# Optimization experiments

Measured on AMD Instinct MI355X. Metric: run time of the kernel, lower is better.

The kernel has to match this reference:

```python
import jax, jax.numpy as jnp
import numpy as np

TOP_K = 2

def setup_inputs() -> dict:
    key = jax.random.key(0)
    ks = jax.random.split(key, 8)
    B, T, C, E, I, S = 1, 2048, 2048, 8, 1408, 2816
    s = 0.02  # weight scale for numerical stability
    return {
        "x": jax.random.normal(ks[0], (B, T, C), jnp.float32),
        "gate_w": jax.random.normal(ks[1], (E, C), jnp.float32) * s,
        "w1": jax.random.normal(ks[2], (E, I, C), jnp.float32) * s,
        "w3": jax.random.normal(ks[3], (E, I, C), jnp.float32) * s,
        "w2": jax.random.normal(ks[4], (E, C, I), jnp.float32) * s,
        "sw1": jax.random.normal(ks[5], (S, C), jnp.float32) * s,
        "sw3": jax.random.normal(ks[6], (S, C), jnp.float32) * s,
        "sw2": jax.random.normal(ks[7], (C, S), jnp.float32) * s,
    }

def reference(x, gate_w, w1, w3, w2, sw1, sw3, sw2):
    B, T, C = x.shape
    E = gate_w.shape[0]
    xf = x.reshape(-1, C)                      # [N, C]
    N = xf.shape[0]
    # --- routing: top-k of raw logits, softmax over the k selected logits ---
    logits = xf @ gate_w.T                     # [N, E]
    pv, idx = jax.lax.top_k(logits, TOP_K)     # [N, K]
    pv = jax.nn.softmax(pv.astype(jnp.float32), axis=-1).astype(x.dtype)
    # token-expert combine weights (sum of probs per expert, scatter of top-k)
    tew = jnp.zeros((N, E), x.dtype).at[jnp.arange(N)[:, None], idx].add(pv)
    # --- experts (SwiGLU), computed densely over all experts and masked by tew ---
    h = jax.nn.silu(jnp.einsum('nc,eic->nei', xf, w1)) * jnp.einsum('nc,eic->nei', xf, w3)
    eo = jnp.einsum('nei,eci->nec', h, w2)     # [N, E, C]
    y = jnp.einsum('nec,ne->nc', eo, tew).reshape(B, T, C)
    # --- shared expert on the residual input ---
    sh = (jax.nn.silu(x @ sw1.T) * (x @ sw3.T)) @ sw2.T
    return y + sh
```

## Files before the change

### kernel.cpp

```cpp
#include <hip/hip_runtime.h>

#define DEVI __device__ __forceinline__

typedef __attribute__((ext_vector_type(4))) float f32x4;
typedef __attribute__((ext_vector_type(8))) short bf16x8;

static constexpr int NT = 2048;
static constexpr int CD = 2048;
static constexpr int NE = 8;
static constexpr int ID = 1408;
static constexpr int SD = 2816;
static constexpr int ROWS = 2 * NT;
static constexpr int ROWS_PAD = ROWS + 128;

DEVI unsigned short f2bf(float f) {
  unsigned u = __builtin_bit_cast(unsigned, f);
  u += 0x7fff + ((u >> 16) & 1);
  return (unsigned short)(u >> 16);
}
DEVI float bf2f(unsigned short s) { return __builtin_bit_cast(float, (unsigned)s << 16); }
DEVI float silu_f(float z) { return z / (1.f + __expf(-z)); }

DEVI void gll16(const void* g, void* l) {
  __builtin_amdgcn_global_load_lds((__attribute__((address_space(1))) void*)(void*)g,
                                   (__attribute__((address_space(3))) void*)l, 16, 0, 0);
}

DEVI void bar_sched() {
  __builtin_amdgcn_s_barrier();
  __builtin_amdgcn_sched_barrier(0);
}
DEVI void wait_vm8() { asm volatile("s_waitcnt vmcnt(8)" ::: "memory"); }
DEVI void wait_vm0() { asm volatile("s_waitcnt vmcnt(0)" ::: "memory"); }
DEVI void wait_lgk0() { asm volatile("s_waitcnt lgkmcnt(0)" ::: "memory"); }

DEVI int swz_chunk(int bid, int nwg) {
  constexpr int CH = 16, G = 8 * CH;
  int nfull = nwg - (nwg % G);
  if (bid >= nfull) return bid;
  int c = bid / G, r = bid % G;
  return c * G + (r % 8) * CH + (r / 8);
}

__global__ __launch_bounds__(256) void k_cvt(const float* __restrict__ s,
                                             unsigned short* __restrict__ d, int n8)
{
  int i = blockIdx.x * 256 + threadIdx.x;
  int stride = gridDim.x * 256;
  for (; i < n8; i += stride) {
    float4 a = ((const float4*)s)[2 * i];
    float4 b = ((const float4*)s)[2 * i + 1];
    ushort4 p0 = make_ushort4(f2bf(a.x), f2bf(a.y), f2bf(a.z), f2bf(a.w));
    ushort4 p1 = make_ushort4(f2bf(b.x), f2bf(b.y), f2bf(b.z), f2bf(b.w));
    ((ushort4*)d)[2 * i]     = p0;
    ((ushort4*)d)[2 * i + 1] = p1;
  }
}

__global__ __launch_bounds__(64) void k_router(const float* __restrict__ x,
    const float* __restrict__ gw, int* __restrict__ counts,
    int* __restrict__ eidx, int* __restrict__ posn, float* __restrict__ probs)
{
  const int n = blockIdx.x;
  const int lane = threadIdx.x;
  const float4* xr = (const float4*)(x + (size_t)n * CD);
  float acc[NE];
#pragma unroll
  for (int e = 0; e < NE; ++e) acc[e] = 0.f;
  for (int i = lane; i < CD / 4; i += 64) {
    float4 xv = xr[i];
#pragma unroll
    for (int e = 0; e < NE; ++e) {
      float4 gv = ((const float4*)(gw + (size_t)e * CD))[i];
      acc[e] += xv.x * gv.x + xv.y * gv.y + xv.z * gv.z + xv.w * gv.w;
    }
  }
#pragma unroll
  for (int e = 0; e < NE; ++e) {
    float v = acc[e];
#pragma unroll
    for (int off = 32; off > 0; off >>= 1) v += __shfl_down(v, off);
    acc[e] = v;
  }
  if (lane == 0) {
    int b0 = 0; float m0 = acc[0];
#pragma unroll
    for (int e = 1; e < NE; ++e) if (acc[e] > m0) { m0 = acc[e]; b0 = e; }
    int b1 = -1; float m1 = 0.f;
#pragma unroll
    for (int e = 0; e < NE; ++e) {
      if (e == b0) continue;
      if (b1 < 0 || acc[e] > m1) { m1 = acc[e]; b1 = e; }
    }
    float d = __expf(m1 - m0);
    float inv = 1.f / (1.f + d);
    eidx[2 * n] = b0; eidx[2 * n + 1] = b1;
    probs[2 * n] = inv; probs[2 * n + 1] = d * inv;
    posn[2 * n] = atomicAdd(&counts[b0], 1);
    posn[2 * n + 1] = atomicAdd(&counts[b1], 1);
  }
}

__global__ void k_scan(const int* __restrict__ counts, int* __restrict__ bases) {
  if (threadIdx.x == 0) {
    int s = 0;
    for (int e = 0; e < NE; ++e) { bases[e] = s; s += counts[e]; }
  }
}

__global__ __launch_bounds__(256) void k_build(const int* __restrict__ eidx,
    const int* __restrict__ posn, const int* __restrict__ bases,
    int* __restrict__ rows_of, int* __restrict__ row2tok)
{
  int n = blockIdx.x * 256 + threadIdx.x;
  if (n >= NT) return;
#pragma unroll
  for (int k = 0; k < 2; ++k) {
    int e = eidx[2 * n + k];
    int row = bases[e] + posn[2 * n + k];
    rows_of[2 * n + k] = row;
    row2tok[row] = n;
  }
}

struct GArgs {
  const unsigned short* A;
  const unsigned short* B1; const unsigned short* B3;
  void* Out;
  const int* counts; const int* bases; const int* row2tok;
  const int* rows_of; const float* probs; const unsigned short* eo;
};

template<int MODE>
__global__ __launch_bounds__(256) void k_gemm(GArgs a)
{
  constexpr bool DUAL = (MODE == 0 || MODE == 2);
  constexpr int KD = (MODE == 0 || MODE == 2) ? CD : (MODE == 1 ? ID : SD);
  constexpr int BN = DUAL ? 64 : 128;
  constexpr int NH = BN / 2;
  constexpr int NFT = NH / 16;
  constexpr int BT = DUAL ? 2 : 4;
  constexpr int NMB = NT / 128;
  constexpr int NPN = (MODE == 0) ? ID / 64 : (MODE == 2) ? SD / 64 : CD / 128;
  constexpr int NWG = NMB * NPN * ((MODE <= 1) ? NE : 1);
  constexpr int NSTEP = KD / 64;

  __shared__ __align__(16) char sm[2][32768];

  int lin = swz_chunk((int)blockIdx.x, NWG);
  const int mx = lin % NMB; lin /= NMB;
  const int pn = lin % NPN;
  const int e  = lin / NPN;

  int M, baserow = 0;
  if constexpr (MODE <= 1) {
    int ne = a.counts[e];
    if (mx * 128 >= ne) return;
    M = ne; baserow = a.bases[e];
  } else { M = NT; }
  const int m0 = mx * 128;
  const int n0 = pn * BN;

  const unsigned short* B1;
  const unsigned short* B3 = nullptr;
  if constexpr (MODE == 0)      { B1 = a.B1 + ((size_t)e * ID + n0) * CD; B3 = a.B3 + ((size_t)e * ID + n0) * CD; }
  else if constexpr (MODE == 1) { B1 = a.B1 + ((size_t)e * CD + n0) * ID; }
  else if constexpr (MODE == 2) { B1 = a.B1 + (size_t)n0 * CD; B3 = a.B3 + (size_t)n0 * CD; }
  else                          { B1 = a.B1 + (size_t)n0 * SD; }

  const int tid = threadIdx.x, l = tid & 63, w = tid >> 6;
  const int wr = w >> 1, wc = w & 1;
  const int slot = ((l & 7) ^ ((l >> 3) & 7)) * 16;

  const char* aP[4];
#pragma unroll
  for (int t = 0; t < 4; ++t) {
    int r = w * 32 + t * 8 + (l >> 3);
    const unsigned short* rb;
    if constexpr (MODE == 0) {
      int grow = m0 + r; int gr = grow < M ? grow : 0;
      rb = a.A + (size_t)a.row2tok[baserow + gr] * CD;
    } else if constexpr (MODE == 1) {
      rb = a.A + (size_t)(baserow + m0 + r) * KD;
    } else {
      rb = a.A + (size_t)(m0 + r) * KD;
    }
    aP[t] = (const char*)rb + slot;
  }
  const char* bP1[BT]; const char* bP3[BT];
#pragma unroll
  for (int t = 0; t < BT; ++t) {
    int r = w * (8 * BT) + t * 8 + (l >> 3);
    bP1[t] = (const char*)(B1 + (size_t)r * KD) + slot;
    if constexpr (DUAL) bP3[t] = (const char*)(B3 + (size_t)r * KD) + slot;
  }

  f32x4 acc1[4][NFT]; f32x4 acc3[4][NFT];
#pragma unroll
  for (int m = 0; m < 4; ++m)
#pragma unroll
    for (int n = 0; n < NFT; ++n) {
      acc1[m][n] = {0.f, 0.f, 0.f, 0.f};
      if constexpr (DUAL) acc3[m][n] = {0.f, 0.f, 0.f, 0.f};
    }

  const int lrow = l & 15, lkg = l >> 4, l7 = l & 7;
  const int ao0 = (lkg ^ l7) * 16;
  const int ao1 = ((4 + lkg) ^ l7) * 16;

  auto stageF = [&](char* base, size_t kb) {
    char* sA = base; char* sB1 = base + 16384; char* sB3 = base + 24576;
#pragma unroll
    for (int t = 0; t < 4; ++t) gll16(aP[t] + kb, sA + (w * 4 + t) * 1024);
#pragma unroll
    for (int t = 0; t < BT; ++t) {
      gll16(bP1[t] + kb, sB1 + (w * BT + t) * 1024);
      if constexpr (DUAL) gll16(bP3[t] + kb, sB3 + (w * BT + t) * 1024);
    }
  };
  auto computeF = [&](const char* base) {
    const char* sA = base; const char* sB1 = base + 16384; const char* sB3 = base + 24576;
#pragma unroll
    for (int kk = 0; kk < 2; ++kk) {
      const int ao = kk ? ao1 : ao0;
      bf16x8 af[4];
#pragma unroll
      for (int m = 0; m < 4; ++m)
        af[m] = *(const bf16x8*)(sA + (wr * 64 + m * 16 + lrow) * 128 + ao);
#pragma unroll
      for (int n = 0; n < NFT; ++n) {
        bf16x8 b1 = *(const bf16x8*)(sB1 + (wc * NH + n * 16 + lrow) * 128 + ao);
        bf16x8 b3;
        if constexpr (DUAL)
          b3 = *(const bf16x8*)(sB3 + (wc * NH + n * 16 + lrow) * 128 + ao);
#pragma unroll
        for (int m = 0; m < 4; ++m) {
          acc1[m][n] = __builtin_amdgcn_mfma_f32_16x16x32_bf16(af[m], b1, acc1[m][n], 0, 0, 0);
          if constexpr (DUAL)
            acc3[m][n] = __builtin_amdgcn_mfma_f32_16x16x32_bf16(af[m], b3, acc3[m][n], 0, 0, 0);
        }
      }
    }
  };

  stageF(sm[0], 0);
  int t = 0;
  for (; t < NSTEP - 2; t += 2) {
    stageF(sm[1], (size_t)(t + 1) * 128);
    wait_vm8(); bar_sched();
    computeF(sm[0]);
    wait_lgk0(); bar_sched();
    stageF(sm[0], (size_t)(t + 2) * 128);
    wait_vm8(); bar_sched();
    computeF(sm[1]);
    wait_lgk0(); bar_sched();
  }
  stageF(sm[1], (size_t)(NSTEP - 1) * 128);
  wait_vm8(); bar_sched();
  computeF(sm[0]);
  wait_vm0(); bar_sched();
  computeF(sm[1]);

#pragma unroll
  for (int m = 0; m < 4; ++m) {
    int rbase = m0 + wr * 64 + m * 16 + lkg * 4;
#pragma unroll
    for (int j = 0; j < 4; ++j) {
      int grow = rbase + j;
      if constexpr (MODE <= 1) { if (grow >= M) continue; }
      int r0 = 0, r1 = 0; float p0 = 0.f, p1 = 0.f;
      if constexpr (MODE == 3) {
        r0 = a.rows_of[2 * grow]; r1 = a.rows_of[2 * grow + 1];
        p0 = a.probs[2 * grow];   p1 = a.probs[2 * grow + 1];
      }
#pragma unroll
      for (int n = 0; n < NFT; ++n) {
        int gcol = n0 + wc * NH + n * 16 + lrow;
        float v1 = acc1[m][n][j];
        if constexpr (MODE == 0) {
          float hh = silu_f(v1) * acc3[m][n][j];
          ((unsigned short*)a.Out)[(size_t)(baserow + grow) * ID + gcol] = f2bf(hh);
        } else if constexpr (MODE == 1) {
          ((unsigned short*)a.Out)[(size_t)(baserow + grow) * CD + gcol] = f2bf(v1);
        } else if constexpr (MODE == 2) {
          float hh = silu_f(v1) * acc3[m][n][j];
          ((unsigned short*)a.Out)[(size_t)grow * SD + gcol] = f2bf(hh);
        } else {
          float vv = v1 + p0 * bf2f(a.eo[(size_t)r0 * CD + gcol]) + p1 * bf2f(a.eo[(size_t)r1 * CD + gcol]);
          ((float*)a.Out)[(size_t)grow * CD + gcol] = vv;
        }
      }
    }
  }
}

extern "C" void kernel_launch(void* const* d_in, const int* in_sizes, int n_in,
                              void* d_out, int out_size, void* d_ws, size_t ws_size,
                              hipStream_t stream)
{
  const float* x   = (const float*)d_in[0];
  const float* gw  = (const float*)d_in[1];
  const float* w1  = (const float*)d_in[2];
  const float* w3  = (const float*)d_in[3];
  const float* w2  = (const float*)d_in[4];
  const float* sw1 = (const float*)d_in[5];
  const float* sw3 = (const float*)d_in[6];
  const float* sw2 = (const float*)d_in[7];
  float* y = (float*)d_out;

  char* p = (char*)d_ws;
  auto alloc = [&](size_t b) { char* r = p; p += (b + 255) & ~(size_t)255; return r; };
  int*   counts  = (int*)alloc(NE * 4);
  int*   bases   = (int*)alloc(NE * 4);
  int*   eidx    = (int*)alloc((size_t)NT * 2 * 4);
  int*   posn    = (int*)alloc((size_t)NT * 2 * 4);
  float* probs   = (float*)alloc((size_t)NT * 2 * 4);
  int*   rows_of = (int*)alloc((size_t)NT * 2 * 4);
  int*   row2tok = (int*)alloc((size_t)ROWS * 4);
  unsigned short* xb   = (unsigned short*)alloc((size_t)NT * CD * 2);
  unsigned short* w1b  = (unsigned short*)alloc((size_t)NE * ID * CD * 2);
  unsigned short* w3b  = (unsigned short*)alloc((size_t)NE * ID * CD * 2);
  unsigned short* w2b  = (unsigned short*)alloc((size_t)NE * CD * ID * 2);
  unsigned short* sw1b = (unsigned short*)alloc((size_t)SD * CD * 2);
  unsigned short* sw3b = (unsigned short*)alloc((size_t)SD * CD * 2);
  unsigned short* sw2b = (unsigned short*)alloc((size_t)CD * SD * 2);
  unsigned short* h    = (unsigned short*)alloc((size_t)ROWS_PAD * ID * 2);
  unsigned short* eo   = (unsigned short*)alloc((size_t)ROWS_PAD * CD * 2);
  unsigned short* hs   = (unsigned short*)alloc((size_t)NT * SD * 2);

  hipMemsetAsync(counts, 0, NE * 4, stream);

  auto cvt = [&](const float* s, unsigned short* d, size_t n) {
    int n8 = (int)(n / 8);
    int grid = (n8 + 255) / 256; if (grid > 2048) grid = 2048;
    k_cvt<<<grid, 256, 0, stream>>>(s, d, n8);
  };
  cvt(x,   xb,   (size_t)NT * CD);
  cvt(w1,  w1b,  (size_t)NE * ID * CD);
  cvt(w3,  w3b,  (size_t)NE * ID * CD);
  cvt(w2,  w2b,  (size_t)NE * CD * ID);
  cvt(sw1, sw1b, (size_t)SD * CD);
  cvt(sw3, sw3b, (size_t)SD * CD);
  cvt(sw2, sw2b, (size_t)CD * SD);

  k_router<<<NT, 64, 0, stream>>>(x, gw, counts, eidx, posn, probs);
  k_scan<<<1, 64, 0, stream>>>(counts, bases);
  k_build<<<NT / 256, 256, 0, stream>>>(eidx, posn, bases, rows_of, row2tok);

  {
    GArgs g{}; g.A = xb; g.B1 = sw1b; g.B3 = sw3b; g.Out = hs;
    k_gemm<2><<<(NT / 128) * (SD / 64), 256, 0, stream>>>(g);
  }
  {
    GArgs g{}; g.A = xb; g.B1 = w1b; g.B3 = w3b; g.Out = h;
    g.counts = counts; g.bases = bases; g.row2tok = row2tok;
    k_gemm<0><<<(NT / 128) * (ID / 64) * NE, 256, 0, stream>>>(g);
  }
  {
    GArgs g{}; g.A = h; g.B1 = w2b; g.Out = eo;
    g.counts = counts; g.bases = bases;
    k_gemm<1><<<(NT / 128) * (CD / 128) * NE, 256, 0, stream>>>(g);
  }
  {
    GArgs g{}; g.A = hs; g.B1 = sw2b; g.Out = y;
    g.rows_of = rows_of; g.probs = probs; g.eo = eo;
    k_gemm<3><<<(NT / 128) * (CD / 128), 256, 0, stream>>>(g);
  }
}
```

Baseline: 401.2 us.

## Merge shared and routed GEMMs into grouped kernels with 256-row tiles

Replaces the four per-mode GEMM launches with two grouped kernels. One handles the shared and routed up-projections together, the other the down-projections. Tiles grow to 256 rows with 512 threads and 128 KB of dynamic LDS, and a separate combine kernel adds the weighted expert outputs into y. The aim is more data reuse per tile, one wave of mixed work to fill the CUs, and less launch and tail overhead. In exchange, expert tiles padded to 256 rows waste more compute, and the extra combine pass rereads y and eo.

```diff
diff --git a/kernel.cpp b/kernel.cpp
--- a/kernel.cpp
+++ b/kernel.cpp
@@ -11,7 +11,7 @@
 static constexpr int ID = 1408;
 static constexpr int SD = 2816;
 static constexpr int ROWS = 2 * NT;
-static constexpr int ROWS_PAD = ROWS + 128;
+static constexpr int ROWS_PAD = ROWS + 256;
 
 DEVI unsigned short f2bf(float f) {
   unsigned u = __builtin_bit_cast(unsigned, f);
@@ -34,8 +34,8 @@
 DEVI void wait_vm0() { asm volatile("s_waitcnt vmcnt(0)" ::: "memory"); }
 DEVI void wait_lgk0() { asm volatile("s_waitcnt lgkmcnt(0)" ::: "memory"); }
 
-DEVI int swz_chunk(int bid, int nwg) {
-  constexpr int CH = 16, G = 8 * CH;
+DEVI int swz8(int bid, int nwg) {
+  constexpr int CH = 8, G = 64;
   int nfull = nwg - (nwg % G);
   if (bid >= nfull) return bid;
   int c = bid / G, r = bid % G;
@@ -123,175 +123,268 @@
   }
 }
 
-struct GArgs {
-  const unsigned short* A;
-  const unsigned short* B1; const unsigned short* B3;
-  void* Out;
-  const int* counts; const int* bases; const int* row2tok;
-  const int* rows_of; const float* probs; const unsigned short* eo;
-};
-
-template<int MODE>
-__global__ __launch_bounds__(256) void k_gemm(GArgs a)
-{
-  constexpr bool DUAL = (MODE == 0 || MODE == 2);
-  constexpr int KD = (MODE == 0 || MODE == 2) ? CD : (MODE == 1 ? ID : SD);
-  constexpr int BN = DUAL ? 64 : 128;
-  constexpr int NH = BN / 2;
-  constexpr int NFT = NH / 16;
-  constexpr int BT = DUAL ? 2 : 4;
-  constexpr int NMB = NT / 128;
-  constexpr int NPN = (MODE == 0) ? ID / 64 : (MODE == 2) ? SD / 64 : CD / 128;
-  constexpr int NWG = NMB * NPN * ((MODE <= 1) ? NE : 1);
-  constexpr int NSTEP = KD / 64;
-
-  __shared__ __align__(16) char sm[2][32768];
-
-  int lin = swz_chunk((int)blockIdx.x, NWG);
-  const int mx = lin % NMB; lin /= NMB;
-  const int pn = lin % NPN;
-  const int e  = lin / NPN;
-
-  int M, baserow = 0;
-  if constexpr (MODE <= 1) {
-    int ne = a.counts[e];
-    if (mx * 128 >= ne) return;
-    M = ne; baserow = a.bases[e];
-  } else { M = NT; }
-  const int m0 = mx * 128;
-  const int n0 = pn * BN;
-
-  const unsigned short* B1;
-  const unsigned short* B3 = nullptr;
-  if constexpr (MODE == 0)      { B1 = a.B1 + ((size_t)e * ID + n0) * CD; B3 = a.B3 + ((size_t)e * ID + n0) * CD; }
-  else if constexpr (MODE == 1) { B1 = a.B1 + ((size_t)e * CD + n0) * ID; }
-  else if constexpr (MODE == 2) { B1 = a.B1 + (size_t)n0 * CD; B3 = a.B3 + (size_t)n0 * CD; }
-  else                          { B1 = a.B1 + (size_t)n0 * SD; }
+__global__ __launch_bounds__(512, 2) void k_up(
+    const unsigned short* __restrict__ xb,
+    const unsigned short* __restrict__ w1b, const unsigned short* __restrict__ w3b,
+    const unsigned short* __restrict__ sw1b, const unsigned short* __restrict__ sw3b,
+    unsigned short* __restrict__ h, unsigned short* __restrict__ hs,
+    const int* __restrict__ counts, const int* __restrict__ bases,
+    const int* __restrict__ row2tok)
+{
+  extern __shared__ char sm[];
+  constexpr int NSH = (NT / 256) * (SD / 128);
+  constexpr int NWG = NSH + NE * (ID / 128) * (NT / 256);
+  constexpr int NSTEP = CD / 64;
+
+  int lin = swz8((int)blockIdx.x, NWG);
+  int cls, mx, pn, e = 0;
+  if (lin < NSH) { cls = 0; mx = lin % 8; pn = lin / 8; }
+  else { cls = 1; int r = lin - NSH; mx = r % 8; r /= 8; pn = r % 11; e = r / 11; }
+
+  int M = NT, baserow = 0;
+  if (cls) { M = counts[e]; if (mx * 256 >= M) return; baserow = bases[e]; }
+  const int m0 = mx * 256, n0 = pn * 128;
+
+  const unsigned short* B1 = cls ? w1b + ((size_t)e * ID + n0) * CD : sw1b + (size_t)n0 * CD;
+  const unsigned short* B3 = cls ? w3b + ((size_t)e * ID + n0) * CD : sw3b + (size_t)n0 * CD;
 
   const int tid = threadIdx.x, l = tid & 63, w = tid >> 6;
-  const int wr = w >> 1, wc = w & 1;
-  const int slot = ((l & 7) ^ ((l >> 3) & 7)) * 16;
+  const int wr = w >> 2, wn = w & 3;
+  const int slot = ((tid & 7) ^ ((tid >> 3) & 7)) * 16;
 
   const char* aP[4];
 #pragma unroll
   for (int t = 0; t < 4; ++t) {
-    int r = w * 32 + t * 8 + (l >> 3);
+    int r = t * 64 + (tid >> 3);
     const unsigned short* rb;
-    if constexpr (MODE == 0) {
+    if (cls) {
       int grow = m0 + r; int gr = grow < M ? grow : 0;
-      rb = a.A + (size_t)a.row2tok[baserow + gr] * CD;
-    } else if constexpr (MODE == 1) {
-      rb = a.A + (size_t)(baserow + m0 + r) * KD;
+      rb = xb + (size_t)row2tok[baserow + gr] * CD;
     } else {
-      rb = a.A + (size_t)(m0 + r) * KD;
+      rb = xb + (size_t)(m0 + r) * CD;
     }
     aP[t] = (const char*)rb + slot;
   }
-  const char* bP1[BT]; const char* bP3[BT];
-#pragma unroll
-  for (int t = 0; t < BT; ++t) {
-    int r = w * (8 * BT) + t * 8 + (l >> 3);
-    bP1[t] = (const char*)(B1 + (size_t)r * KD) + slot;
-    if constexpr (DUAL) bP3[t] = (const char*)(B3 + (size_t)r * KD) + slot;
-  }
-
-  f32x4 acc1[4][NFT]; f32x4 acc3[4][NFT];
-#pragma unroll
-  for (int m = 0; m < 4; ++m)
-#pragma unroll
-    for (int n = 0; n < NFT; ++n) {
+  const char* bP1[2]; const char* bP3[2];
+#pragma unroll
+  for (int t = 0; t < 2; ++t) {
+    int r = t * 64 + (tid >> 3);
+    bP1[t] = (const char*)(B1 + (size_t)r * CD) + slot;
+    bP3[t] = (const char*)(B3 + (size_t)r * CD) + slot;
+  }
+
+  f32x4 acc1[8][2], acc3[8][2];
+#pragma unroll
+  for (int m = 0; m < 8; ++m)
+#pragma unroll
+    for (int n = 0; n < 2; ++n) {
       acc1[m][n] = {0.f, 0.f, 0.f, 0.f};
-      if constexpr (DUAL) acc3[m][n] = {0.f, 0.f, 0.f, 0.f};
+      acc3[m][n] = {0.f, 0.f, 0.f, 0.f};
     }
 
   const int lrow = l & 15, lkg = l >> 4, l7 = l & 7;
-  const int ao0 = (lkg ^ l7) * 16;
-  const int ao1 = ((4 + lkg) ^ l7) * 16;
+  const int ao0 = (lkg ^ l7) * 16, ao1 = ((4 + lkg) ^ l7) * 16;
 
   auto stageF = [&](char* base, size_t kb) {
-    char* sA = base; char* sB1 = base + 16384; char* sB3 = base + 24576;
-#pragma unroll
-    for (int t = 0; t < 4; ++t) gll16(aP[t] + kb, sA + (w * 4 + t) * 1024);
-#pragma unroll
-    for (int t = 0; t < BT; ++t) {
-      gll16(bP1[t] + kb, sB1 + (w * BT + t) * 1024);
-      if constexpr (DUAL) gll16(bP3[t] + kb, sB3 + (w * BT + t) * 1024);
+    char* sA = base; char* sB1 = base + 32768; char* sB3 = base + 49152;
+#pragma unroll
+    for (int t = 0; t < 4; ++t) gll16(aP[t] + kb, sA + t * 8192 + tid * 16);
+#pragma unroll
+    for (int t = 0; t < 2; ++t) {
+      gll16(bP1[t] + kb, sB1 + t * 8192 + tid * 16);
+      gll16(bP3[t] + kb, sB3 + t * 8192 + tid * 16);
     }
   };
   auto computeF = [&](const char* base) {
-    const char* sA = base; const char* sB1 = base + 16384; const char* sB3 = base + 24576;
+    const char* sA = base; const char* sB1 = base + 32768; const char* sB3 = base + 49152;
 #pragma unroll
     for (int kk = 0; kk < 2; ++kk) {
       const int ao = kk ? ao1 : ao0;
-      bf16x8 af[4];
-#pragma unroll
-      for (int m = 0; m < 4; ++m)
-        af[m] = *(const bf16x8*)(sA + (wr * 64 + m * 16 + lrow) * 128 + ao);
-#pragma unroll
-      for (int n = 0; n < NFT; ++n) {
-        bf16x8 b1 = *(const bf16x8*)(sB1 + (wc * NH + n * 16 + lrow) * 128 + ao);
-        bf16x8 b3;
-        if constexpr (DUAL)
-          b3 = *(const bf16x8*)(sB3 + (wc * NH + n * 16 + lrow) * 128 + ao);
-#pragma unroll
-        for (int m = 0; m < 4; ++m) {
+      bf16x8 af[8];
+#pragma unroll
+      for (int m = 0; m < 8; ++m)
+        af[m] = *(const bf16x8*)(sA + (wr * 128 + m * 16 + lrow) * 128 + ao);
+#pragma unroll
+      for (int n = 0; n < 2; ++n) {
+        bf16x8 b1 = *(const bf16x8*)(sB1 + (wn * 32 + n * 16 + lrow) * 128 + ao);
+        bf16x8 b3 = *(const bf16x8*)(sB3 + (wn * 32 + n * 16 + lrow) * 128 + ao);
+#pragma unroll
+        for (int m = 0; m < 8; ++m) {
           acc1[m][n] = __builtin_amdgcn_mfma_f32_16x16x32_bf16(af[m], b1, acc1[m][n], 0, 0, 0);
-          if constexpr (DUAL)
-            acc3[m][n] = __builtin_amdgcn_mfma_f32_16x16x32_bf16(af[m], b3, acc3[m][n], 0, 0, 0);
+          acc3[m][n] = __builtin_amdgcn_mfma_f32_16x16x32_bf16(af[m], b3, acc3[m][n], 0, 0, 0);
         }
       }
     }
   };
 
-  stageF(sm[0], 0);
+  char* s0 = sm; char* s1 = sm + 65536;
+  stageF(s0, 0);
   int t = 0;
   for (; t < NSTEP - 2; t += 2) {
-    stageF(sm[1], (size_t)(t + 1) * 128);
+    stageF(s1, (size_t)(t + 1) * 128);
     wait_vm8(); bar_sched();
-    computeF(sm[0]);
+    computeF(s0);
     wait_lgk0(); bar_sched();
-    stageF(sm[0], (size_t)(t + 2) * 128);
+    stageF(s0, (size_t)(t + 2) * 128);
     wait_vm8(); bar_sched();
-    computeF(sm[1]);
+    computeF(s1);
     wait_lgk0(); bar_sched();
   }
-  stageF(sm[1], (size_t)(NSTEP - 1) * 128);
+  stageF(s1, (size_t)(NSTEP - 1) * 128);
   wait_vm8(); bar_sched();
-  computeF(sm[0]);
+  computeF(s0);
   wait_vm0(); bar_sched();
-  computeF(sm[1]);
-
-#pragma unroll
-  for (int m = 0; m < 4; ++m) {
-    int rbase = m0 + wr * 64 + m * 16 + lkg * 4;
+  computeF(s1);
+
+#pragma unroll
+  for (int m = 0; m < 8; ++m) {
+    int rb_ = m0 + wr * 128 + m * 16 + lkg * 4;
 #pragma unroll
     for (int j = 0; j < 4; ++j) {
-      int grow = rbase + j;
-      if constexpr (MODE <= 1) { if (grow >= M) continue; }
-      int r0 = 0, r1 = 0; float p0 = 0.f, p1 = 0.f;
-      if constexpr (MODE == 3) {
-        r0 = a.rows_of[2 * grow]; r1 = a.rows_of[2 * grow + 1];
-        p0 = a.probs[2 * grow];   p1 = a.probs[2 * grow + 1];
+      int grow = rb_ + j;
+      if (cls && grow >= M) continue;
+#pragma unroll
+      for (int n = 0; n < 2; ++n) {
+        int gcol = n0 + wn * 32 + n * 16 + lrow;
+        float hh = silu_f(acc1[m][n][j]) * acc3[m][n][j];
+        if (cls) h[(size_t)(baserow + grow) * ID + gcol] = f2bf(hh);
+        else     hs[(size_t)grow * SD + gcol] = f2bf(hh);
       }
-#pragma unroll
-      for (int n = 0; n < NFT; ++n) {
-        int gcol = n0 + wc * NH + n * 16 + lrow;
-        float v1 = acc1[m][n][j];
-        if constexpr (MODE == 0) {
-          float hh = silu_f(v1) * acc3[m][n][j];
-          ((unsigned short*)a.Out)[(size_t)(baserow + grow) * ID + gcol] = f2bf(hh);
-        } else if constexpr (MODE == 1) {
-          ((unsigned short*)a.Out)[(size_t)(baserow + grow) * CD + gcol] = f2bf(v1);
-        } else if constexpr (MODE == 2) {
-          float hh = silu_f(v1) * acc3[m][n][j];
-          ((unsigned short*)a.Out)[(size_t)grow * SD + gcol] = f2bf(hh);
-        } else {
-          float vv = v1 + p0 * bf2f(a.eo[(size_t)r0 * CD + gcol]) + p1 * bf2f(a.eo[(size_t)r1 * CD + gcol]);
-          ((float*)a.Out)[(size_t)grow * CD + gcol] = vv;
-        }
+    }
+  }
+}
+
+__global__ __launch_bounds__(512, 2) void k_down(
+    const unsigned short* __restrict__ h, const unsigned short* __restrict__ hs,
+    const unsigned short* __restrict__ w2b, const unsigned short* __restrict__ sw2b,
+    unsigned short* __restrict__ eo, float* __restrict__ y,
+    const int* __restrict__ counts, const int* __restrict__ bases)
+{
+  extern __shared__ char sm[];
+  constexpr int NRT = NE * (CD / 256) * (NT / 256);
+  constexpr int NWG = NRT + (CD / 256) * (NT / 256);
+
+  int lin = swz8((int)blockIdx.x, NWG);
+  int cls, mx, pn, e = 0;
+  if (lin < NRT) { cls = 1; mx = lin % 8; int r = lin / 8; pn = r % 8; e = r / 8; }
+  else { cls = 0; int r = lin - NRT; mx = r % 8; pn = r / 8; }
+
+  int M = NT, baserow = 0;
+  if (cls) { M = counts[e]; if (mx * 256 >= M) return; baserow = bases[e]; }
+  const int m0 = mx * 256, n0 = pn * 256;
+  const int KD_ = cls ? ID : SD;
+  const int nstep = KD_ / 64;
+
+  const unsigned short* B = cls ? w2b + ((size_t)e * CD + n0) * ID : sw2b + (size_t)n0 * SD;
+
+  const int tid = threadIdx.x, l = tid & 63, w = tid >> 6;
+  const int wr = w >> 2, wn = w & 3;
+  const int slot = ((tid & 7) ^ ((tid >> 3) & 7)) * 16;
+
+  const char* aP[4]; const char* bP[4];
+#pragma unroll
+  for (int t = 0; t < 4; ++t) {
+    int r = t * 64 + (tid >> 3);
+    const unsigned short* rb = cls ? h + (size_t)(baserow + m0 + r) * ID
+                                   : hs + (size_t)(m0 + r) * SD;
+    aP[t] = (const char*)rb + slot;
+    bP[t] = (const char*)(B + (size_t)r * KD_) + slot;
+  }
+
+  f32x4 acc[8][4];
+#pragma unroll
+  for (int m = 0; m < 8; ++m)
+#pragma unroll
+    for (int n = 0; n < 4; ++n) acc[m][n] = {0.f, 0.f, 0.f, 0.f};
+
+  const int lrow = l & 15, lkg = l >> 4, l7 = l & 7;
+  const int ao0 = (lkg ^ l7) * 16, ao1 = ((4 + lkg) ^ l7) * 16;
+
+  auto stageF = [&](char* base, size_t kb) {
+    char* sA = base; char* sB = base + 32768;
+#pragma unroll
+    for (int t = 0; t < 4; ++t) {
+      gll16(aP[t] + kb, sA + t * 8192 + tid * 16);
+      gll16(bP[t] + kb, sB + t * 8192 + tid * 16);
+    }
+  };
+  auto computeF = [&](const char* base) {
+    const char* sA = base; const char* sB = base + 32768;
+#pragma unroll
+    for (int kk = 0; kk < 2; ++kk) {
+      const int ao = kk ? ao1 : ao0;
+      bf16x8 af[8];
+#pragma unroll
+      for (int m = 0; m < 8; ++m)
+        af[m] = *(const bf16x8*)(sA + (wr * 128 + m * 16 + lrow) * 128 + ao);
+#pragma unroll
+      for (int n = 0; n < 4; ++n) {
+        bf16x8 bv = *(const bf16x8*)(sB + (wn * 64 + n * 16 + lrow) * 128 + ao);
+#pragma unroll
+        for (int m = 0; m < 8; ++m)
+          acc[m][n] = __builtin_amdgcn_mfma_f32_16x16x32_bf16(af[m], bv, acc[m][n], 0, 0, 0);
       }
     }
-  }
+  };
+
+  char* s0 = sm; char* s1 = sm + 65536;
+  stageF(s0, 0);
+  int t = 0;
+  for (; t < nstep - 2; t += 2) {
+    stageF(s1, (size_t)(t + 1) * 128);
+    wait_vm8(); bar_sched();
+    computeF(s0);
+    wait_lgk0(); bar_sched();
+    stageF(s0, (size_t)(t + 2) * 128);
+    wait_vm8(); bar_sched();
+    computeF(s1);
+    wait_lgk0(); bar_sched();
+  }
+  stageF(s1, (size_t)(nstep - 1) * 128);
+  wait_vm8(); bar_sched();
+  computeF(s0);
+  wait_vm0(); bar_sched();
+  computeF(s1);
+
+#pragma unroll
+  for (int m = 0; m < 8; ++m) {
+    int rb_ = m0 + wr * 128 + m * 16 + lkg * 4;
+#pragma unroll
+    for (int j = 0; j < 4; ++j) {
+      int grow = rb_ + j;
+      if (cls && grow >= M) continue;
+#pragma unroll
+      for (int n = 0; n < 4; ++n) {
+        int gcol = n0 + wn * 64 + n * 16 + lrow;
+        float v = acc[m][n][j];
+        if (cls) eo[(size_t)(baserow + grow) * CD + gcol] = f2bf(v);
+        else     y[(size_t)grow * CD + gcol] = v;
+      }
+    }
+  }
+}
+
+__global__ __launch_bounds__(256) void k_combine(float* __restrict__ y,
+    const unsigned short* __restrict__ eo, const int* __restrict__ rows_of,
+    const float* __restrict__ probs)
+{
+  const int n = blockIdx.x;
+  const int c = threadIdx.x * 8;
+  const int r0 = rows_of[2 * n], r1 = rows_of[2 * n + 1];
+  const float p0 = probs[2 * n], p1 = probs[2 * n + 1];
+  bf16x8 e0 = *(const bf16x8*)(eo + (size_t)r0 * CD + c);
+  bf16x8 e1 = *(const bf16x8*)(eo + (size_t)r1 * CD + c);
+  float* yp = y + (size_t)n * CD + c;
+  float4 y0 = *(float4*)yp, y1 = *(float4*)(yp + 4);
+  y0.x += p0 * bf2f((unsigned short)e0[0]) + p1 * bf2f((unsigned short)e1[0]);
+  y0.y += p0 * bf2f((unsigned short)e0[1]) + p1 * bf2f((unsigned short)e1[1]);
+  y0.z += p0 * bf2f((unsigned short)e0[2]) + p1 * bf2f((unsigned short)e1[2]);
+  y0.w += p0 * bf2f((unsigned short)e0[3]) + p1 * bf2f((unsigned short)e1[3]);
+  y1.x += p0 * bf2f((unsigned short)e0[4]) + p1 * bf2f((unsigned short)e1[4]);
+  y1.y += p0 * bf2f((unsigned short)e0[5]) + p1 * bf2f((unsigned short)e1[5]);
+  y1.z += p0 * bf2f((unsigned short)e0[6]) + p1 * bf2f((unsigned short)e1[6]);
+  y1.w += p0 * bf2f((unsigned short)e0[7]) + p1 * bf2f((unsigned short)e1[7]);
+  *(float4*)yp = y0; *(float4*)(yp + 4) = y1;
 }
 
 extern "C" void kernel_launch(void* const* d_in, const int* in_sizes, int n_in,
@@ -328,6 +421,9 @@
   unsigned short* eo   = (unsigned short*)alloc((size_t)ROWS_PAD * CD * 2);
   unsigned short* hs   = (unsigned short*)alloc((size_t)NT * SD * 2);
 
+  hipFuncSetAttribute((const void*)k_up,   hipFuncAttributeMaxDynamicSharedMemorySize, 131072);
+  hipFuncSetAttribute((const void*)k_down, hipFuncAttributeMaxDynamicSharedMemorySize, 131072);
+
   hipMemsetAsync(counts, 0, NE * 4, stream);
 
   auto cvt = [&](const float* s, unsigned short* d, size_t n) {
@@ -348,22 +444,13 @@
   k_build<<<NT / 256, 256, 0, stream>>>(eidx, posn, bases, rows_of, row2tok);
 
   {
-    GArgs g{}; g.A = xb; g.B1 = sw1b; g.B3 = sw3b; g.Out = hs;
-    k_gemm<2><<<(NT / 128) * (SD / 64), 256, 0, stream>>>(g);
+    constexpr int NWG = (NT / 256) * (SD / 128) + NE * (ID / 128) * (NT / 256);
+    k_up<<<NWG, 512, 131072, stream>>>(xb, w1b, w3b, sw1b, sw3b, h, hs,
+                                       counts, bases, row2tok);
   }
   {
-    GArgs g{}; g.A = xb; g.B1 = w1b; g.B3 = w3b; g.Out = h;
-    g.counts = counts; g.bases = bases; g.row2tok = row2tok;
-    k_gemm<0><<<(NT / 128) * (ID / 64) * NE, 256, 0, stream>>>(g);
-  }
-  {
-    GArgs g{}; g.A = h; g.B1 = w2b; g.Out = eo;
-    g.counts = counts; g.bases = bases;
-    k_gemm<1><<<(NT / 128) * (CD / 128) * NE, 256, 0, stream>>>(g);
-  }
-  {
-    GArgs g{}; g.A = hs; g.B1 = sw2b; g.Out = y;
-    g.rows_of = rows_of; g.probs = probs; g.eo = eo;
-    k_gemm<3><<<(NT / 128) * (CD / 128), 256, 0, stream>>>(g);
-  }
-}
+    constexpr int NWG = NE * (CD / 256) * (NT / 256) + (CD / 256) * (NT / 256);
+    k_down<<<NWG, 512, 131072, stream>>>(h, hs, w2b, sw2b, eo, y, counts, bases);
+  }
+  k_combine<<<NT, 256, 0, stream>>>(y, eo, rows_of, probs);
+}
```

Measured after the change: 468.9 us. +16.9%, slower.
